# Kernel optimization log

Measured on AMD Instinct MI355X. Metric: run time of the kernel, lower is better.

Reference implementation:

```python
import jax, jax.numpy as jnp
import numpy as np

B, S, T, E, H = 16, 96, 50, 128, 128
D2 = 2 * H
V = 32000
NGRAM = 2
ALPHA = 0.25


def _lstm(x, Wih, Whh, b, reverse=False):
    # x: [N, T, E] -> outputs [N, T, H], final h, c (PyTorch gate order i,f,g,o)
    xt = jnp.swapaxes(x, 0, 1)
    if reverse:
        xt = xt[::-1]
    n = x.shape[0]
    h = Whh.shape[1]
    init = (jnp.zeros((n, h), x.dtype), jnp.zeros((n, h), x.dtype))

    def step(carry, xin):
        hprev, cprev = carry
        g = xin @ Wih.T + hprev @ Whh.T + b
        i, f, gg, o = jnp.split(g, 4, axis=-1)
        c = jax.nn.sigmoid(f) * cprev + jax.nn.sigmoid(i) * jnp.tanh(gg)
        hnew = jax.nn.sigmoid(o) * jnp.tanh(c)
        return (hnew, c), hnew

    (hT, cT), outs = jax.lax.scan(step, init, xt)
    if reverse:
        outs = outs[::-1]
    return jnp.swapaxes(outs, 0, 1), hT, cT


def _gru(x, h, Wi, Wh, bi, bh):
    # PyTorch GRUCell, gate order r,z,n
    gi = x @ Wi.T + bi
    gh = h @ Wh.T + bh
    ir, iz, inn = jnp.split(gi, 3, axis=-1)
    hr, hz, hn = jnp.split(gh, 3, axis=-1)
    r = jax.nn.sigmoid(ir + hr)
    z = jax.nn.sigmoid(iz + hz)
    n = jnp.tanh(inn + r * hn)
    return (1.0 - z) * n + z * h


def _norm_scale(x):
    # (||x|| + alpha) / (||x|| + 1), detached as in the original
    v = jnp.linalg.norm(x, axis=1)
    return jax.lax.stop_gradient(((v + ALPHA) / (v + 1.0))[:, None])


def setup_inputs() -> dict:
    key = jax.random.key(0)
    ks = jax.random.split(key, 30)
    rn = lambda k, sh: jax.random.normal(k, sh, jnp.float32) * 0.05
    return {
        "enc_batch": jax.random.randint(ks[0], (B * S, T), 0, V),
        "struct_parent": jax.random.randint(ks[1], (B, S, S), 0, B * S + 1),
        "struct_child": jax.random.randint(ks[2], (B, S, S), 0, B * S + 1),
        "mask_emb": (jax.random.uniform(ks[3], (B, S, S, 1)) < 0.2).astype(jnp.float32),
        "emb_table": rn(ks[4], (V, E)),
        "Wih_f": rn(ks[5], (4 * H, E)), "Whh_f": rn(ks[6], (4 * H, H)), "b_f": rn(ks[7], (4 * H,)),
        "Wih_b": rn(ks[8], (4 * H, E)), "Whh_b": rn(ks[9], (4 * H, H)), "b_b": rn(ks[10], (4 * H,)),
        "Wc": rn(ks[11], (H, D2)), "bc": rn(ks[12], (H,)),
        "Whr": rn(ks[13], (H, D2)), "bhr": rn(ks[14], (H,)),
        "Wi_cp": rn(ks[15], (3 * D2, D2)), "Wh_cp": rn(ks[16], (3 * D2, D2)),
        "bi_cp": rn(ks[17], (3 * D2,)), "bh_cp": rn(ks[18], (3 * D2,)),
        "Wi_pc": rn(ks[19], (3 * D2, D2)), "Wh_pc": rn(ks[20], (3 * D2, D2)),
        "bi_pc": rn(ks[21], (3 * D2,)), "bh_pc": rn(ks[22], (3 * D2,)),
    }


def reference(enc_batch, struct_parent, struct_child, mask_emb, emb_table,
              Wih_f, Whh_f, b_f, Wih_b, Whh_b, b_b, Wc, bc, Whr, bhr,
              Wi_cp, Wh_cp, bi_cp, bh_cp, Wi_pc, Wh_pc, bi_pc, bh_pc):
    # Sentence encoder (bidirectional LSTM); dropout=0 -> identity
    emb = emb_table[enc_batch]                       # [B*S, T, E]
    _, hf, cf = _lstm(emb, Wih_f, Whh_f, b_f)
    _, hb, cb = _lstm(emb, Wih_b, Whh_b, b_b, reverse=True)
    c_red = jax.nn.relu(jnp.concatenate([cf, cb], 1) @ Wc.T + bc)
    h_red = jax.nn.relu(jnp.concatenate([hf, hb], 1) @ Whr.T + bhr)
    enc_states = jnp.concatenate([c_red, h_red], 1)  # [B*S, 2H]
    zero = jnp.zeros((1, D2), enc_states.dtype)
    hidden = jnp.concatenate([zero, enc_states], 0)  # [B*S+1, 2H]; row 0 = zero_emb

    # child -> parent message passing
    for _ in range(NGRAM):
        p = hidden[struct_parent].reshape(-1, D2)    # gather [B*S*S, 2H]
        c = hidden[struct_child].reshape(-1, D2)
        ch = _gru(c, p, Wi_cp, Wh_cp, bi_cp, bh_cp).reshape(B, S, S, D2)
        ch = (ch * mask_emb).sum(1).reshape(B * S, D2)
        ch = jnp.concatenate([zero, ch], 0)
        hidden = hidden + ch * _norm_scale(ch)

    # parent -> child message passing
    for _ in range(NGRAM):
        p = hidden[struct_parent].reshape(-1, D2)
        c = hidden[struct_child].reshape(-1, D2)
        ch = _gru(p, c, Wi_pc, Wh_pc, bi_pc, bh_pc).reshape(B, S, S, D2)
        ch = (ch * mask_emb).sum(2).reshape(B * S, D2)
        ch = jnp.concatenate([zero, ch], 0)
        hidden = hidden + ch * _norm_scale(ch)

    return hidden
```

## Files before the change

kernel.cpp:

```cpp
#include <hip/hip_runtime.h>

typedef unsigned short u16;
typedef __attribute__((ext_vector_type(8))) short bf8;
typedef __attribute__((ext_vector_type(4))) short s16x4;
typedef __attribute__((ext_vector_type(4))) float f32x4;
typedef __attribute__((ext_vector_type(4))) int   i32x4;
typedef __attribute__((ext_vector_type(2))) int   i32x2;

#define S_   96
#define T_   50
#define NSEQ 1536
#define NR   1537
#define XROW 520

__device__ __forceinline__ float bf2f(u16 u){ return __uint_as_float(((unsigned)u)<<16); }
__device__ __forceinline__ u16 f2bf(float f){
  unsigned u = __float_as_uint(f);
  u += 0x7fffu + ((u>>16)&1u);
  return (u16)(u>>16);
}
__device__ __forceinline__ int cvtpk(float lo, float hi){
  int r; asm("v_cvt_pk_bf16_f32 %0, %1, %2" : "=v"(r) : "v"(lo), "v"(hi)); return r;
}
__device__ __forceinline__ float sigm(float x){
  return __builtin_amdgcn_rcpf(1.f + __expf(-x));
}
__device__ __forceinline__ float tanh_(float x){
  return 1.f - 2.f*__builtin_amdgcn_rcpf(__expf(2.f*x) + 1.f);
}
__device__ __forceinline__ void bar_lds(){
  asm volatile("s_waitcnt lgkmcnt(0)\n\ts_barrier" ::: "memory");
}

struct CvtArgs { const float* s[10]; u16* d[10]; };
__global__ __launch_bounds__(256) void prep_kernel(CvtArgs a,
    const int* __restrict__ par, const int* __restrict__ chi,
    const float* __restrict__ mask,
    int2* __restrict__ ent0, int* __restrict__ cnt0,
    int2* __restrict__ ent1, int* __restrict__ cnt1)
{
  if (blockIdx.x < 1088){
    int e = (blockIdx.x*256 + threadIdx.x)*4;
    if (e >= 1114112) return;
    int t, off;
    if (e < 262144){ t = e>>16; off = e & 65535; }
    else if (e < 327680){ int e2=e-262144; t = 4+(e2>>15); off = e2&32767; }
    else { int e3=e-327680; t = 6 + e3/196608; off = e3%196608; }
    int src = off;
    if (t < 4){
      int colp = off>>7, k = off&127;
      int orig = ((colp>>4)&3)*128 + ((colp>>6)<<4) + (colp&15);
      src = orig*128 + k;
    }
    f32x4 v = *reinterpret_cast<const f32x4*>(a.s[t]+src);
    i32x2 o;
    o[0] = cvtpk(v[0], v[1]);
    o[1] = cvtpk(v[2], v[3]);
    *reinterpret_cast<i32x2*>(a.d[t]+off) = o;
  } else {
    const int rr = blockIdx.x - 1088;
    __shared__ int c0s, c1s;
    if (threadIdx.x==0){ c0s=0; c1s=0; }
    __syncthreads();
    const int l = threadIdx.x;
    if (l < S_){
      const int b = rr/S_, fx = rr%S_, base = b*S_*S_;
      int idx = base + l*S_ + fx;
      if (mask[idx] != 0.f){
        int p = atomicAdd(&c0s, 1);
        ent0[rr*S_ + p] = make_int2(chi[idx], par[idx]);
      }
      int jdx = base + fx*S_ + l;
      if (mask[jdx] != 0.f){
        int p = atomicAdd(&c1s, 1);
        ent1[rr*S_ + p] = make_int2(par[jdx], chi[jdx]);
      }
    }
    __syncthreads();
    if (threadIdx.x==0){ cnt0[rr]=c0s; cnt1[rr]=c1s; }
  }
}

__global__ __launch_bounds__(512, 2) void lstm_kernel(
    const int* __restrict__ enc, const float* __restrict__ emb,
    const u16* __restrict__ WihF, const u16* __restrict__ WhhF, const float* __restrict__ bF,
    const u16* __restrict__ WihB, const u16* __restrict__ WhhB, const float* __restrict__ bB,
    u16* __restrict__ c_cat, u16* __restrict__ h_cat)
{
  __shared__ short xh[16*XROW];
  __shared__ int   toks[16*T_];

  const int tid  = threadIdx.x;
  const int wave = tid>>6;
  const int lane = tid&63;
  const int dir  = blockIdx.y;
  const int s0   = blockIdx.x*16;

  const u16* Wih = dir ? WihB : WihF;
  const u16* Whh = dir ? WhhB : WhhF;
  const float* bb = dir ? bB  : bF;

  for (int i=tid; i<16*T_; i+=512)
    toks[i] = enc[(s0 + i/T_)*T_ + (i%T_)];

  const int mL   = lane&15;
  const int quad = lane>>4;
  const int kb   = quad*8;

  bf8 Breg[4][8];
  f32x4 bias4[4];
  #pragma unroll
  for (int n=0;n<4;n++){
    int colp = wave*64 + n*16 + mL;
    bias4[n] = *reinterpret_cast<const f32x4*>(bb + n*128 + wave*16 + quad*4);
    #pragma unroll
    for (int ks=0;ks<8;ks++){
      int k = ks*32 + kb;
      const u16* p = (k<128) ? (Wih + colp*128 + k) : (Whh + colp*128 + (k-128));
      Breg[n][ks] = *reinterpret_cast<const bf8*>(p);
      asm volatile("" : "+v"(Breg[n][ks]));
    }
  }

  if (tid<256){
    int r = tid>>4, c = tid&15;
    *reinterpret_cast<i32x4*>(&xh[r*XROW + 256 + c*8]) = (i32x4){0,0,0,0};
  }

  const int srow = tid>>5, schunk = tid&31;
  float cst[4] = {0.f,0.f,0.f,0.f};
  float hst[4] = {0.f,0.f,0.f,0.f};

  __syncthreads();

  {
    int tok0 = toks[srow*T_ + (dir ? (T_-1) : 0)];
    f32x4 x0 = *reinterpret_cast<const f32x4*>(emb + tok0*128 + schunk*4);
    int tok1 = toks[srow*T_ + (dir ? (T_-2) : 1)];
    f32x4 x1 = *reinterpret_cast<const f32x4*>(emb + tok1*128 + schunk*4);
    i32x2 p0; p0[0]=cvtpk(x0[0],x0[1]); p0[1]=cvtpk(x0[2],x0[3]);
    i32x2 p1; p1[0]=cvtpk(x1[0],x1[1]); p1[1]=cvtpk(x1[2],x1[3]);
    *reinterpret_cast<i32x2*>(&xh[srow*XROW +       schunk*4]) = p0;
    *reinterpret_cast<i32x2*>(&xh[srow*XROW + 128 + schunk*4]) = p1;
  }
  f32x4 xvA, xvB;
  {
    int tA = toks[srow*T_ + (dir ? (T_-3) : 2)];
    xvA = *reinterpret_cast<const f32x4*>(emb + tA*128 + schunk*4);
    int tB = toks[srow*T_ + (dir ? (T_-4) : 3)];
    xvB = *reinterpret_cast<const f32x4*>(emb + tB*128 + schunk*4);
  }
  __syncthreads();

  f32x4 accx[4];
  #pragma unroll
  for (int n=0;n<4;n++) accx[n] = (f32x4){0.f,0.f,0.f,0.f};
  #pragma unroll
  for (int ks=0;ks<4;ks++){
    bf8 b = *reinterpret_cast<const bf8*>(&xh[mL*XROW + ks*32 + kb]);
    #pragma unroll
    for (int n=0;n<4;n++)
      accx[n] = __builtin_amdgcn_mfma_f32_16x16x32_bf16(Breg[n][ks], b, accx[n], 0,0,0);
  }
  bar_lds();

  for (int t=0;t<T_;t++){
    const int cb = t&1, nb = cb^1;

    f32x4 acc[4];
    #pragma unroll
    for (int n=0;n<4;n++) acc[n] = accx[n];
    #pragma unroll
    for (int ks=0;ks<4;ks++){
      bf8 b = *reinterpret_cast<const bf8*>(&xh[mL*XROW + 256 + cb*128 + ks*32 + kb]);
      #pragma unroll
      for (int n=0;n<4;n++)
        acc[n] = __builtin_amdgcn_mfma_f32_16x16x32_bf16(Breg[n][4+ks], b, acc[n], 0,0,0);
    }

    if (t+2 < T_){
      i32x2 p; p[0]=cvtpk(xvA[0],xvA[1]); p[1]=cvtpk(xvA[2],xvA[3]);
      *reinterpret_cast<i32x2*>(&xh[srow*XROW + cb*128 + schunk*4]) = p;
    }
    xvA = xvB;
    if (t+4 < T_){
      int tok = toks[srow*T_ + (dir ? (T_-5-t) : (t+4))];
      xvB = *reinterpret_cast<const f32x4*>(emb + tok*128 + schunk*4);
    }

    if (t+1 < T_){
      #pragma unroll
      for (int n=0;n<4;n++) accx[n] = (f32x4){0.f,0.f,0.f,0.f};
      #pragma unroll
      for (int ks=0;ks<4;ks++){
        bf8 b = *reinterpret_cast<const bf8*>(&xh[mL*XROW + nb*128 + ks*32 + kb]);
        #pragma unroll
        for (int n=0;n<4;n++)
          accx[n] = __builtin_amdgcn_mfma_f32_16x16x32_bf16(Breg[n][ks], b, accx[n], 0,0,0);
      }
    }

    float hv4[4];
    #pragma unroll
    for (int i=0;i<4;i++){
      float gi_ = acc[0][i]+bias4[0][i];
      float gf_ = acc[1][i]+bias4[1][i];
      float gg_ = acc[2][i]+bias4[2][i];
      float go_ = acc[3][i]+bias4[3][i];
      float c = sigm(gf_)*cst[i] + sigm(gi_)*tanh_(gg_);
      float h = sigm(go_)*tanh_(c);
      cst[i]=c; hst[i]=h; hv4[i]=h;
    }
    i32x2 hp;
    hp[0]=cvtpk(hv4[0],hv4[1]); hp[1]=cvtpk(hv4[2],hv4[3]);
    *reinterpret_cast<i32x2*>(&xh[mL*XROW + 256 + nb*128 + wave*16 + quad*4]) = hp;
    bar_lds();
  }

  {
    const int ch = wave*16 + quad*4;
    const int gs = s0 + mL;
    i32x2 cp_, hp_;
    cp_[0]=cvtpk(cst[0],cst[1]); cp_[1]=cvtpk(cst[2],cst[3]);
    hp_[0]=cvtpk(hst[0],hst[1]); hp_[1]=cvtpk(hst[2],hst[3]);
    *reinterpret_cast<i32x2*>(c_cat + gs*256 + dir*128 + ch) = cp_;
    *reinterpret_cast<i32x2*>(h_cat + gs*256 + dir*128 + ch) = hp_;
  }
}

__global__ __launch_bounds__(256) void reduce_kernel(
    const u16* __restrict__ c_cat, const u16* __restrict__ h_cat,
    const u16* __restrict__ Wc, const float* __restrict__ bc,
    const u16* __restrict__ Whr, const float* __restrict__ bhr,
    float* __restrict__ hidf, u16* __restrict__ hidb)
{
  const int tid=threadIdx.x, wave=tid>>6, lane=tid&63;
  const int mL=lane&15, quad=lane>>4, kb=quad*8;
  const int m0 = blockIdx.x*64;
  const u16* A    = (wave<2) ? c_cat : h_cat;
  const u16* W    = (wave<2) ? Wc  : Whr;
  const float* bv = (wave<2) ? bc  : bhr;
  const int nb    = (wave&1)*64;
  const int obase = (wave<2) ? 0 : 128;

  f32x4 acc[4][4];
  #pragma unroll
  for (int mt=0;mt<4;mt++)
    #pragma unroll
    for (int nt=0;nt<4;nt++) acc[mt][nt] = (f32x4){0.f,0.f,0.f,0.f};

  #pragma unroll
  for (int ks=0;ks<8;ks++){
    int k = ks*32 + kb;
    bf8 bfr[4];
    #pragma unroll
    for (int nt=0;nt<4;nt++)
      bfr[nt] = *reinterpret_cast<const bf8*>(W + (nb+nt*16+mL)*256 + k);
    #pragma unroll
    for (int mt=0;mt<4;mt++){
      bf8 a = *reinterpret_cast<const bf8*>(A + (m0+mt*16+mL)*256 + k);
      #pragma unroll
      for (int nt=0;nt<4;nt++)
        acc[mt][nt] = __builtin_amdgcn_mfma_f32_16x16x32_bf16(a, bfr[nt], acc[mt][nt], 0,0,0);
    }
  }
  const int row0 = quad*4;
  float biasv[4];
  #pragma unroll
  for (int nt=0;nt<4;nt++) biasv[nt] = bv[nb+nt*16+mL];
  #pragma unroll
  for (int mt=0;mt<4;mt++){
    #pragma unroll
    for (int nt=0;nt<4;nt++){
      int col = obase + nb + nt*16 + mL;
      #pragma unroll
      for (int i=0;i<4;i++){
        int r = m0 + mt*16 + row0 + i;
        float v = fmaxf(acc[mt][nt][i] + biasv[nt], 0.f);
        hidf[(r+1)*256 + col] = v;
        hidb[(r+1)*256 + col] = f2bf(v);
      }
    }
  }
  if (blockIdx.x==0 && tid<64){
    #pragma unroll
    for (int j=0;j<4;j++){ hidf[tid*4+j] = 0.f; hidb[tid*4+j] = 0; }
  }
}

__global__ __launch_bounds__(256) void gates_gemm_kernel(
    const u16* __restrict__ hidb,
    const u16* __restrict__ Wi, const u16* __restrict__ Wh,
    const float* __restrict__ bi, const float* __restrict__ bh,
    u16* __restrict__ gi, u16* __restrict__ gh)
{
  const int tid=threadIdx.x, wave=tid>>6, lane=tid&63;
  const int mL=lane&15, quad=lane>>4, kb=quad*8;
  const int m0 = blockIdx.x*32;
  const int n0 = blockIdx.y*256 + wave*64;
  const bool isI = (n0 < 768);
  const u16* W    = isI ? Wi : Wh;
  const float* bv = isI ? bi : bh;
  u16* out        = isI ? gi : gh;
  const int nbc   = isI ? n0 : (n0-768);

  int arow[2];
  #pragma unroll
  for (int mt=0;mt<2;mt++) arow[mt] = min(m0+mt*16+mL, NR-1);

  f32x4 acc[2][4];
  #pragma unroll
  for (int mt=0;mt<2;mt++)
    #pragma unroll
    for (int nt=0;nt<4;nt++) acc[mt][nt] = (f32x4){0.f,0.f,0.f,0.f};

  #pragma unroll
  for (int ks=0;ks<8;ks++){
    int k = ks*32 + kb;
    bf8 bfr[4];
    #pragma unroll
    for (int nt=0;nt<4;nt++)
      bfr[nt] = *reinterpret_cast<const bf8*>(W + (nbc+nt*16+mL)*256 + k);
    #pragma unroll
    for (int mt=0;mt<2;mt++){
      bf8 a = *reinterpret_cast<const bf8*>(hidb + arow[mt]*256 + k);
      #pragma unroll
      for (int nt=0;nt<4;nt++)
        acc[mt][nt] = __builtin_amdgcn_mfma_f32_16x16x32_bf16(a, bfr[nt], acc[mt][nt], 0,0,0);
    }
  }
  const int row0 = quad*4;
  float biasv[4];
  #pragma unroll
  for (int nt=0;nt<4;nt++) biasv[nt] = bv[nbc+nt*16+mL];
  #pragma unroll
  for (int mt=0;mt<2;mt++){
    #pragma unroll
    for (int nt=0;nt<4;nt++){
      #pragma unroll
      for (int i=0;i<4;i++){
        int r = m0 + mt*16 + row0 + i;
        if (r < NR)
          out[r*768 + nbc + nt*16 + mL] = f2bf(acc[mt][nt][i] + biasv[nt]);
      }
    }
  }
}

__global__ __launch_bounds__(512) void pair_kernel(
    const u16* __restrict__ gi, const u16* __restrict__ gh,
    const float* __restrict__ hin,
    float* __restrict__ hout, u16* __restrict__ bout, float* __restrict__ dout,
    const int2* __restrict__ ent, const int* __restrict__ cnt)
{
  const int r = blockIdx.x;
  const int tid = threadIdx.x, wave = tid>>6, lane = tid&63;
  __shared__ float part[8][260];
  __shared__ float ssum[4];
  if (r==0){
    if (tid<256){
      hout[tid]=0.f; bout[tid]=0;
      if (dout) dout[tid]=0.f;
    }
    return;
  }
  const int rr = r-1;
  const int n  = cnt[rr];
  const int2* e = ent + rr*S_;
  const int ch0 = lane*4;

  float a0=0.f, a1=0.f, a2=0.f, a3=0.f;
  for (int k=wave; k<n; k+=8){
    int2 pr = e[k];
    const u16* gx = gi + pr.x*768 + ch0;
    const u16* gy = gh + pr.y*768 + ch0;
    s16x4 vi0 = *reinterpret_cast<const s16x4*>(gx);
    s16x4 vi1 = *reinterpret_cast<const s16x4*>(gx+256);
    s16x4 vi2 = *reinterpret_cast<const s16x4*>(gx+512);
    s16x4 vh0 = *reinterpret_cast<const s16x4*>(gy);
    s16x4 vh1 = *reinterpret_cast<const s16x4*>(gy+256);
    s16x4 vh2 = *reinterpret_cast<const s16x4*>(gy+512);
    f32x4 hv  = *reinterpret_cast<const f32x4*>(hin + pr.y*256 + ch0);
    float o[4];
    #pragma unroll
    for (int i=0;i<4;i++){
      float rg = sigm(bf2f((u16)vi0[i]) + bf2f((u16)vh0[i]));
      float zg = sigm(bf2f((u16)vi1[i]) + bf2f((u16)vh1[i]));
      float ng = tanh_(bf2f((u16)vi2[i]) + rg*bf2f((u16)vh2[i]));
      o[i] = (1.f-zg)*ng + zg*hv[i];
    }
    a0 += o[0]; a1 += o[1]; a2 += o[2]; a3 += o[3];
  }
  *reinterpret_cast<f32x4*>(&part[wave][ch0]) = (f32x4){a0,a1,a2,a3};
  __syncthreads();

  if (tid < 256){
    float tot = part[0][tid] + part[1][tid] + part[2][tid] + part[3][tid]
              + part[4][tid] + part[5][tid] + part[6][tid] + part[7][tid];
    part[0][tid] = tot;
    float sq = tot*tot;
    #pragma unroll
    for (int off=32; off>0; off>>=1) sq += __shfl_xor(sq, off, 64);
    if (lane==0) ssum[wave] = sq;
  }
  __syncthreads();
  if (tid < 256){
    float tot = part[0][tid];
    float v  = sqrtf(ssum[0]+ssum[1]+ssum[2]+ssum[3]);
    float sc = (v + 0.25f)*__builtin_amdgcn_rcpf(v + 1.f);
    float nv = hin[r*256 + tid] + tot*sc;
    hout[r*256 + tid] = nv;
    bout[r*256 + tid] = f2bf(nv);
    if (dout) dout[r*256 + tid] = nv;
  }
}

extern "C" void kernel_launch(void* const* d_in, const int* in_sizes, int n_in,
                              void* d_out, int out_size, void* d_ws, size_t ws_size,
                              hipStream_t stream)
{
  const int*   enc  = (const int*)  d_in[0];
  const int*   spar = (const int*)  d_in[1];
  const int*   schi = (const int*)  d_in[2];
  const float* mask = (const float*)d_in[3];
  const float* emb  = (const float*)d_in[4];
  const float* WihF = (const float*)d_in[5];
  const float* WhhF = (const float*)d_in[6];
  const float* bF   = (const float*)d_in[7];
  const float* WihB = (const float*)d_in[8];
  const float* WhhB = (const float*)d_in[9];
  const float* bB   = (const float*)d_in[10];
  const float* Wc   = (const float*)d_in[11];
  const float* bc   = (const float*)d_in[12];
  const float* Whr  = (const float*)d_in[13];
  const float* bhr  = (const float*)d_in[14];
  const float* WiCP = (const float*)d_in[15];
  const float* WhCP = (const float*)d_in[16];
  const float* biCP = (const float*)d_in[17];
  const float* bhCP = (const float*)d_in[18];
  const float* WiPC = (const float*)d_in[19];
  const float* WhPC = (const float*)d_in[20];
  const float* biPC = (const float*)d_in[21];
  const float* bhPC = (const float*)d_in[22];

  char* ws = (char*)d_ws;
  u16*   c_cat = (u16*)  (ws + 0);
  u16*   h_cat = (u16*)  (ws + 786432);
  float* hf0   = (float*)(ws + 1572864);
  float* hf1   = (float*)(ws + 3146752);
  u16*   hb    = (u16*)  (ws + 4720640);
  u16*   gi    = (u16*)  (ws + 5507584);
  u16*   gh    = (u16*)  (ws + 7868416);
  u16*   wbf   = (u16*)  (ws + 10229248);
  int2*  ent0  = (int2*) (ws + 12457472);
  int2*  ent1  = (int2*) (ws + 13637120);
  int*   cnt0  = (int*)  (ws + 14816768);
  int*   cnt1  = (int*)  (ws + 14822912);
  float* out   = (float*)d_out;

  u16* bWihF = wbf + 0;
  u16* bWhhF = wbf + 65536;
  u16* bWihB = wbf + 131072;
  u16* bWhhB = wbf + 196608;
  u16* bWc   = wbf + 262144;
  u16* bWhr  = wbf + 294912;
  u16* bWiCP = wbf + 327680;
  u16* bWhCP = wbf + 524288;
  u16* bWiPC = wbf + 720896;
  u16* bWhPC = wbf + 917504;

  CvtArgs ca;
  ca.s[0]=WihF; ca.s[1]=WhhF; ca.s[2]=WihB; ca.s[3]=WhhB;
  ca.s[4]=Wc;   ca.s[5]=Whr;
  ca.s[6]=WiCP; ca.s[7]=WhCP; ca.s[8]=WiPC; ca.s[9]=WhPC;
  ca.d[0]=bWihF; ca.d[1]=bWhhF; ca.d[2]=bWihB; ca.d[3]=bWhhB;
  ca.d[4]=bWc;   ca.d[5]=bWhr;
  ca.d[6]=bWiCP; ca.d[7]=bWhCP; ca.d[8]=bWiPC; ca.d[9]=bWhPC;
  prep_kernel<<<dim3(1088+NSEQ), dim3(256), 0, stream>>>(
      ca, spar, schi, mask, ent0, cnt0, ent1, cnt1);

  lstm_kernel<<<dim3(96,2), dim3(512), 0, stream>>>(
      enc, emb, bWihF,bWhhF,bF, bWihB,bWhhB,bB, c_cat, h_cat);
  reduce_kernel<<<dim3(24), dim3(256), 0, stream>>>(
      c_cat,h_cat, bWc,bc,bWhr,bhr, hf0,hb);

  float* hfb[2] = {hf0,hf1};
  int cur = 0;
  for (int it=0; it<4; it++){
    const u16* Wi   = (it<2)?bWiCP:bWiPC;
    const u16* Wh   = (it<2)?bWhCP:bWhPC;
    const float* bi = (it<2)?biCP:biPC;
    const float* bh = (it<2)?bhCP:bhPC;
    int nxt = cur^1;
    gates_gemm_kernel<<<dim3(49,6), dim3(256), 0, stream>>>(
        hb, Wi,Wh,bi,bh, gi,gh);
    pair_kernel<<<dim3(NR), dim3(512), 0, stream>>>(
        gi,gh, hfb[cur], hfb[nxt], hb,
        (it==3)?out:(float*)nullptr,
        (it<2)?ent0:ent1, (it<2)?cnt0:cnt1);
    cur = nxt;
  }
}
```

Measured before the change: 322.2 us.

## Merge forward and backward LSTM directions into one 1024-thread block

```diff
diff --git a/kernel.cpp b/kernel.cpp
--- a/kernel.cpp
+++ b/kernel.cpp
@@ -81,26 +81,29 @@
   }
 }
 
-__global__ __launch_bounds__(512, 2) void lstm_kernel(
+__global__ __launch_bounds__(1024, 4) void lstm_kernel(
     const int* __restrict__ enc, const float* __restrict__ emb,
     const u16* __restrict__ WihF, const u16* __restrict__ WhhF, const float* __restrict__ bF,
     const u16* __restrict__ WihB, const u16* __restrict__ WhhB, const float* __restrict__ bB,
     u16* __restrict__ c_cat, u16* __restrict__ h_cat)
 {
-  __shared__ short xh[16*XROW];
+  __shared__ short xh[32*XROW];
   __shared__ int   toks[16*T_];
 
   const int tid  = threadIdx.x;
   const int wave = tid>>6;
   const int lane = tid&63;
-  const int dir  = blockIdx.y;
+  const int dir  = wave>>3;
+  const int w8   = wave&7;
   const int s0   = blockIdx.x*16;
+
+  short* X = xh + dir*16*XROW;
 
   const u16* Wih = dir ? WihB : WihF;
   const u16* Whh = dir ? WhhB : WhhF;
   const float* bb = dir ? bB  : bF;
 
-  for (int i=tid; i<16*T_; i+=512)
+  for (int i=tid; i<16*T_; i+=1024)
     toks[i] = enc[(s0 + i/T_)*T_ + (i%T_)];
 
   const int mL   = lane&15;
@@ -111,8 +114,8 @@
   f32x4 bias4[4];
   #pragma unroll
   for (int n=0;n<4;n++){
-    int colp = wave*64 + n*16 + mL;
-    bias4[n] = *reinterpret_cast<const f32x4*>(bb + n*128 + wave*16 + quad*4);
+    int colp = w8*64 + n*16 + mL;
+    bias4[n] = *reinterpret_cast<const f32x4*>(bb + n*128 + w8*16 + quad*4);
     #pragma unroll
     for (int ks=0;ks<8;ks++){
       int k = ks*32 + kb;
@@ -122,12 +125,13 @@
     }
   }
 
-  if (tid<256){
-    int r = tid>>4, c = tid&15;
-    *reinterpret_cast<i32x4*>(&xh[r*XROW + 256 + c*8]) = (i32x4){0,0,0,0};
-  }
-
-  const int srow = tid>>5, schunk = tid&31;
+  if (tid<512){
+    int d2 = tid>>8, r = (tid>>4)&15, c = tid&15;
+    *reinterpret_cast<i32x4*>(&xh[d2*16*XROW + r*XROW + 256 + c*8]) = (i32x4){0,0,0,0};
+  }
+
+  const int tid9   = tid & 511;
+  const int srow   = tid9>>5, schunk = tid9&31;
   float cst[4] = {0.f,0.f,0.f,0.f};
   float hst[4] = {0.f,0.f,0.f,0.f};
 
@@ -140,8 +144,8 @@
     f32x4 x1 = *reinterpret_cast<const f32x4*>(emb + tok1*128 + schunk*4);
     i32x2 p0; p0[0]=cvtpk(x0[0],x0[1]); p0[1]=cvtpk(x0[2],x0[3]);
     i32x2 p1; p1[0]=cvtpk(x1[0],x1[1]); p1[1]=cvtpk(x1[2],x1[3]);
-    *reinterpret_cast<i32x2*>(&xh[srow*XROW +       schunk*4]) = p0;
-    *reinterpret_cast<i32x2*>(&xh[srow*XROW + 128 + schunk*4]) = p1;
+    *reinterpret_cast<i32x2*>(&X[srow*XROW +       schunk*4]) = p0;
+    *reinterpret_cast<i32x2*>(&X[srow*XROW + 128 + schunk*4]) = p1;
   }
   f32x4 xvA, xvB;
   {
@@ -157,7 +161,7 @@
   for (int n=0;n<4;n++) accx[n] = (f32x4){0.f,0.f,0.f,0.f};
   #pragma unroll
   for (int ks=0;ks<4;ks++){
-    bf8 b = *reinterpret_cast<const bf8*>(&xh[mL*XROW + ks*32 + kb]);
+    bf8 b = *reinterpret_cast<const bf8*>(&X[mL*XROW + ks*32 + kb]);
     #pragma unroll
     for (int n=0;n<4;n++)
       accx[n] = __builtin_amdgcn_mfma_f32_16x16x32_bf16(Breg[n][ks], b, accx[n], 0,0,0);
@@ -172,7 +176,7 @@
     for (int n=0;n<4;n++) acc[n] = accx[n];
     #pragma unroll
     for (int ks=0;ks<4;ks++){
-      bf8 b = *reinterpret_cast<const bf8*>(&xh[mL*XROW + 256 + cb*128 + ks*32 + kb]);
+      bf8 b = *reinterpret_cast<const bf8*>(&X[mL*XROW + 256 + cb*128 + ks*32 + kb]);
       #pragma unroll
       for (int n=0;n<4;n++)
         acc[n] = __builtin_amdgcn_mfma_f32_16x16x32_bf16(Breg[n][4+ks], b, acc[n], 0,0,0);
@@ -180,7 +184,7 @@
 
     if (t+2 < T_){
       i32x2 p; p[0]=cvtpk(xvA[0],xvA[1]); p[1]=cvtpk(xvA[2],xvA[3]);
-      *reinterpret_cast<i32x2*>(&xh[srow*XROW + cb*128 + schunk*4]) = p;
+      *reinterpret_cast<i32x2*>(&X[srow*XROW + cb*128 + schunk*4]) = p;
     }
     xvA = xvB;
     if (t+4 < T_){
@@ -193,7 +197,7 @@
       for (int n=0;n<4;n++) accx[n] = (f32x4){0.f,0.f,0.f,0.f};
       #pragma unroll
       for (int ks=0;ks<4;ks++){
-        bf8 b = *reinterpret_cast<const bf8*>(&xh[mL*XROW + nb*128 + ks*32 + kb]);
+        bf8 b = *reinterpret_cast<const bf8*>(&X[mL*XROW + nb*128 + ks*32 + kb]);
         #pragma unroll
         for (int n=0;n<4;n++)
           accx[n] = __builtin_amdgcn_mfma_f32_16x16x32_bf16(Breg[n][ks], b, accx[n], 0,0,0);
@@ -213,12 +217,12 @@
     }
     i32x2 hp;
     hp[0]=cvtpk(hv4[0],hv4[1]); hp[1]=cvtpk(hv4[2],hv4[3]);
-    *reinterpret_cast<i32x2*>(&xh[mL*XROW + 256 + nb*128 + wave*16 + quad*4]) = hp;
+    *reinterpret_cast<i32x2*>(&X[mL*XROW + 256 + nb*128 + w8*16 + quad*4]) = hp;
     bar_lds();
   }
 
   {
-    const int ch = wave*16 + quad*4;
+    const int ch = w8*16 + quad*4;
     const int gs = s0 + mL;
     i32x2 cp_, hp_;
     cp_[0]=cvtpk(cst[0],cst[1]); cp_[1]=cvtpk(cst[2],cst[3]);
@@ -479,7 +483,7 @@
   prep_kernel<<<dim3(1088+NSEQ), dim3(256), 0, stream>>>(
       ca, spar, schi, mask, ent0, cnt0, ent1, cnt1);
 
-  lstm_kernel<<<dim3(96,2), dim3(512), 0, stream>>>(
+  lstm_kernel<<<dim3(96), dim3(1024), 0, stream>>>(
       enc, emb, bWihF,bWhhF,bF, bWihB,bWhhB,bB, c_cat, h_cat);
   reduce_kernel<<<dim3(24), dim3(256), 0, stream>>>(
       c_cat,h_cat, bWc,bc,bWhr,bhr, hf0,hb);
```

Measured after the change: 758.9 us. +135.5%, slower.

## Process 32 sequences per LSTM block with two interleaved MFMA tiles

Applied to the files above, without the earlier changes.

```diff
diff --git a/kernel.cpp b/kernel.cpp
--- a/kernel.cpp
+++ b/kernel.cpp
@@ -87,20 +87,20 @@
     const u16* __restrict__ WihB, const u16* __restrict__ WhhB, const float* __restrict__ bB,
     u16* __restrict__ c_cat, u16* __restrict__ h_cat)
 {
-  __shared__ short xh[16*XROW];
-  __shared__ int   toks[16*T_];
+  __shared__ short xh[32*XROW];
+  __shared__ int   toks[32*T_];
 
   const int tid  = threadIdx.x;
   const int wave = tid>>6;
   const int lane = tid&63;
   const int dir  = blockIdx.y;
-  const int s0   = blockIdx.x*16;
+  const int s0   = blockIdx.x*32;
 
   const u16* Wih = dir ? WihB : WihF;
   const u16* Whh = dir ? WhhB : WhhF;
   const float* bb = dir ? bB  : bF;
 
-  for (int i=tid; i<16*T_; i+=512)
+  for (int i=tid; i<32*T_; i+=512)
     toks[i] = enc[(s0 + i/T_)*T_ + (i%T_)];
 
   const int mL   = lane&15;
@@ -122,109 +122,153 @@
     }
   }
 
-  if (tid<256){
+  {
     int r = tid>>4, c = tid&15;
     *reinterpret_cast<i32x4*>(&xh[r*XROW + 256 + c*8]) = (i32x4){0,0,0,0};
   }
 
-  const int srow = tid>>5, schunk = tid&31;
-  float cst[4] = {0.f,0.f,0.f,0.f};
-  float hst[4] = {0.f,0.f,0.f,0.f};
+  const int srow = tid>>4, sch = tid&15;
+  float cst0[4] = {0.f,0.f,0.f,0.f}, hst0[4] = {0.f,0.f,0.f,0.f};
+  float cst1[4] = {0.f,0.f,0.f,0.f}, hst1[4] = {0.f,0.f,0.f,0.f};
 
   __syncthreads();
 
   {
     int tok0 = toks[srow*T_ + (dir ? (T_-1) : 0)];
-    f32x4 x0 = *reinterpret_cast<const f32x4*>(emb + tok0*128 + schunk*4);
+    f32x4 a0 = *reinterpret_cast<const f32x4*>(emb + tok0*128 + sch*8);
+    f32x4 a1 = *reinterpret_cast<const f32x4*>(emb + tok0*128 + sch*8 + 4);
     int tok1 = toks[srow*T_ + (dir ? (T_-2) : 1)];
-    f32x4 x1 = *reinterpret_cast<const f32x4*>(emb + tok1*128 + schunk*4);
-    i32x2 p0; p0[0]=cvtpk(x0[0],x0[1]); p0[1]=cvtpk(x0[2],x0[3]);
-    i32x2 p1; p1[0]=cvtpk(x1[0],x1[1]); p1[1]=cvtpk(x1[2],x1[3]);
-    *reinterpret_cast<i32x2*>(&xh[srow*XROW +       schunk*4]) = p0;
-    *reinterpret_cast<i32x2*>(&xh[srow*XROW + 128 + schunk*4]) = p1;
-  }
-  f32x4 xvA, xvB;
+    f32x4 b0 = *reinterpret_cast<const f32x4*>(emb + tok1*128 + sch*8);
+    f32x4 b1 = *reinterpret_cast<const f32x4*>(emb + tok1*128 + sch*8 + 4);
+    i32x4 p0, p1;
+    p0[0]=cvtpk(a0[0],a0[1]); p0[1]=cvtpk(a0[2],a0[3]);
+    p0[2]=cvtpk(a1[0],a1[1]); p0[3]=cvtpk(a1[2],a1[3]);
+    p1[0]=cvtpk(b0[0],b0[1]); p1[1]=cvtpk(b0[2],b0[3]);
+    p1[2]=cvtpk(b1[0],b1[1]); p1[3]=cvtpk(b1[2],b1[3]);
+    *reinterpret_cast<i32x4*>(&xh[srow*XROW +       sch*8]) = p0;
+    *reinterpret_cast<i32x4*>(&xh[srow*XROW + 128 + sch*8]) = p1;
+  }
+  f32x4 xvA0, xvA1, xvB0, xvB1;
   {
     int tA = toks[srow*T_ + (dir ? (T_-3) : 2)];
-    xvA = *reinterpret_cast<const f32x4*>(emb + tA*128 + schunk*4);
+    xvA0 = *reinterpret_cast<const f32x4*>(emb + tA*128 + sch*8);
+    xvA1 = *reinterpret_cast<const f32x4*>(emb + tA*128 + sch*8 + 4);
     int tB = toks[srow*T_ + (dir ? (T_-4) : 3)];
-    xvB = *reinterpret_cast<const f32x4*>(emb + tB*128 + schunk*4);
+    xvB0 = *reinterpret_cast<const f32x4*>(emb + tB*128 + sch*8);
+    xvB1 = *reinterpret_cast<const f32x4*>(emb + tB*128 + sch*8 + 4);
   }
   __syncthreads();
 
-  f32x4 accx[4];
-  #pragma unroll
-  for (int n=0;n<4;n++) accx[n] = (f32x4){0.f,0.f,0.f,0.f};
+  f32x4 accx0[4], accx1[4];
+  #pragma unroll
+  for (int n=0;n<4;n++){ accx0[n] = (f32x4){0.f,0.f,0.f,0.f};
+                         accx1[n] = (f32x4){0.f,0.f,0.f,0.f}; }
   #pragma unroll
   for (int ks=0;ks<4;ks++){
-    bf8 b = *reinterpret_cast<const bf8*>(&xh[mL*XROW + ks*32 + kb]);
-    #pragma unroll
-    for (int n=0;n<4;n++)
-      accx[n] = __builtin_amdgcn_mfma_f32_16x16x32_bf16(Breg[n][ks], b, accx[n], 0,0,0);
+    bf8 b0 = *reinterpret_cast<const bf8*>(&xh[ mL     *XROW + ks*32 + kb]);
+    bf8 b1 = *reinterpret_cast<const bf8*>(&xh[(16+mL)*XROW + ks*32 + kb]);
+    #pragma unroll
+    for (int n=0;n<4;n++){
+      accx0[n] = __builtin_amdgcn_mfma_f32_16x16x32_bf16(Breg[n][ks], b0, accx0[n], 0,0,0);
+      accx1[n] = __builtin_amdgcn_mfma_f32_16x16x32_bf16(Breg[n][ks], b1, accx1[n], 0,0,0);
+    }
   }
   bar_lds();
 
   for (int t=0;t<T_;t++){
     const int cb = t&1, nb = cb^1;
 
-    f32x4 acc[4];
-    #pragma unroll
-    for (int n=0;n<4;n++) acc[n] = accx[n];
+    f32x4 acc0[4], acc1[4];
+    #pragma unroll
+    for (int n=0;n<4;n++){ acc0[n] = accx0[n]; acc1[n] = accx1[n]; }
     #pragma unroll
     for (int ks=0;ks<4;ks++){
-      bf8 b = *reinterpret_cast<const bf8*>(&xh[mL*XROW + 256 + cb*128 + ks*32 + kb]);
-      #pragma unroll
-      for (int n=0;n<4;n++)
-        acc[n] = __builtin_amdgcn_mfma_f32_16x16x32_bf16(Breg[n][4+ks], b, acc[n], 0,0,0);
+      bf8 b0 = *reinterpret_cast<const bf8*>(&xh[ mL     *XROW + 256 + cb*128 + ks*32 + kb]);
+      bf8 b1 = *reinterpret_cast<const bf8*>(&xh[(16+mL)*XROW + 256 + cb*128 + ks*32 + kb]);
+      #pragma unroll
+      for (int n=0;n<4;n++){
+        acc0[n] = __builtin_amdgcn_mfma_f32_16x16x32_bf16(Breg[n][4+ks], b0, acc0[n], 0,0,0);
+        acc1[n] = __builtin_amdgcn_mfma_f32_16x16x32_bf16(Breg[n][4+ks], b1, acc1[n], 0,0,0);
+      }
     }
 
     if (t+2 < T_){
-      i32x2 p; p[0]=cvtpk(xvA[0],xvA[1]); p[1]=cvtpk(xvA[2],xvA[3]);
-      *reinterpret_cast<i32x2*>(&xh[srow*XROW + cb*128 + schunk*4]) = p;
-    }
-    xvA = xvB;
+      i32x4 p;
+      p[0]=cvtpk(xvA0[0],xvA0[1]); p[1]=cvtpk(xvA0[2],xvA0[3]);
+      p[2]=cvtpk(xvA1[0],xvA1[1]); p[3]=cvtpk(xvA1[2],xvA1[3]);
+      *reinterpret_cast<i32x4*>(&xh[srow*XROW + cb*128 + sch*8]) = p;
+    }
+    xvA0 = xvB0; xvA1 = xvB1;
     if (t+4 < T_){
       int tok = toks[srow*T_ + (dir ? (T_-5-t) : (t+4))];
-      xvB = *reinterpret_cast<const f32x4*>(emb + tok*128 + schunk*4);
+      xvB0 = *reinterpret_cast<const f32x4*>(emb + tok*128 + sch*8);
+      xvB1 = *reinterpret_cast<const f32x4*>(emb + tok*128 + sch*8 + 4);
     }
 
     if (t+1 < T_){
       #pragma unroll
-      for (int n=0;n<4;n++) accx[n] = (f32x4){0.f,0.f,0.f,0.f};
+      for (int n=0;n<4;n++){ accx0[n] = (f32x4){0.f,0.f,0.f,0.f};
+                             accx1[n] = (f32x4){0.f,0.f,0.f,0.f}; }
       #pragma unroll
       for (int ks=0;ks<4;ks++){
-        bf8 b = *reinterpret_cast<const bf8*>(&xh[mL*XROW + nb*128 + ks*32 + kb]);
+        bf8 b0 = *reinterpret_cast<const bf8*>(&xh[ mL     *XROW + nb*128 + ks*32 + kb]);
+        bf8 b1 = *reinterpret_cast<const bf8*>(&xh[(16+mL)*XROW + nb*128 + ks*32 + kb]);
         #pragma unroll
-        for (int n=0;n<4;n++)
-          accx[n] = __builtin_amdgcn_mfma_f32_16x16x32_bf16(Breg[n][ks], b, accx[n], 0,0,0);
-      }
-    }
-
-    float hv4[4];
-    #pragma unroll
-    for (int i=0;i<4;i++){
-      float gi_ = acc[0][i]+bias4[0][i];
-      float gf_ = acc[1][i]+bias4[1][i];
-      float gg_ = acc[2][i]+bias4[2][i];
-      float go_ = acc[3][i]+bias4[3][i];
-      float c = sigm(gf_)*cst[i] + sigm(gi_)*tanh_(gg_);
-      float h = sigm(go_)*tanh_(c);
-      cst[i]=c; hst[i]=h; hv4[i]=h;
-    }
-    i32x2 hp;
-    hp[0]=cvtpk(hv4[0],hv4[1]); hp[1]=cvtpk(hv4[2],hv4[3]);
-    *reinterpret_cast<i32x2*>(&xh[mL*XROW + 256 + nb*128 + wave*16 + quad*4]) = hp;
+        for (int n=0;n<4;n++){
+          accx0[n] = __builtin_amdgcn_mfma_f32_16x16x32_bf16(Breg[n][ks], b0, accx0[n], 0,0,0);
+          accx1[n] = __builtin_amdgcn_mfma_f32_16x16x32_bf16(Breg[n][ks], b1, accx1[n], 0,0,0);
+        }
+      }
+    }
+
+    {
+      float hv4[4];
+      #pragma unroll
+      for (int i=0;i<4;i++){
+        float gi_ = acc0[0][i]+bias4[0][i];
+        float gf_ = acc0[1][i]+bias4[1][i];
+        float gg_ = acc0[2][i]+bias4[2][i];
+        float go_ = acc0[3][i]+bias4[3][i];
+        float c = sigm(gf_)*cst0[i] + sigm(gi_)*tanh_(gg_);
+        float h = sigm(go_)*tanh_(c);
+        cst0[i]=c; hst0[i]=h; hv4[i]=h;
+      }
+      i32x2 hp;
+      hp[0]=cvtpk(hv4[0],hv4[1]); hp[1]=cvtpk(hv4[2],hv4[3]);
+      *reinterpret_cast<i32x2*>(&xh[mL*XROW + 256 + nb*128 + wave*16 + quad*4]) = hp;
+    }
+    {
+      float hv4[4];
+      #pragma unroll
+      for (int i=0;i<4;i++){
+        float gi_ = acc1[0][i]+bias4[0][i];
+        float gf_ = acc1[1][i]+bias4[1][i];
+        float gg_ = acc1[2][i]+bias4[2][i];
+        float go_ = acc1[3][i]+bias4[3][i];
+        float c = sigm(gf_)*cst1[i] + sigm(gi_)*tanh_(gg_);
+        float h = sigm(go_)*tanh_(c);
+        cst1[i]=c; hst1[i]=h; hv4[i]=h;
+      }
+      i32x2 hp;
+      hp[0]=cvtpk(hv4[0],hv4[1]); hp[1]=cvtpk(hv4[2],hv4[3]);
+      *reinterpret_cast<i32x2*>(&xh[(16+mL)*XROW + 256 + nb*128 + wave*16 + quad*4]) = hp;
+    }
     bar_lds();
   }
 
   {
     const int ch = wave*16 + quad*4;
-    const int gs = s0 + mL;
     i32x2 cp_, hp_;
-    cp_[0]=cvtpk(cst[0],cst[1]); cp_[1]=cvtpk(cst[2],cst[3]);
-    hp_[0]=cvtpk(hst[0],hst[1]); hp_[1]=cvtpk(hst[2],hst[3]);
-    *reinterpret_cast<i32x2*>(c_cat + gs*256 + dir*128 + ch) = cp_;
-    *reinterpret_cast<i32x2*>(h_cat + gs*256 + dir*128 + ch) = hp_;
+    int gs0 = s0 + mL;
+    cp_[0]=cvtpk(cst0[0],cst0[1]); cp_[1]=cvtpk(cst0[2],cst0[3]);
+    hp_[0]=cvtpk(hst0[0],hst0[1]); hp_[1]=cvtpk(hst0[2],hst0[3]);
+    *reinterpret_cast<i32x2*>(c_cat + gs0*256 + dir*128 + ch) = cp_;
+    *reinterpret_cast<i32x2*>(h_cat + gs0*256 + dir*128 + ch) = hp_;
+    int gs1 = s0 + 16 + mL;
+    cp_[0]=cvtpk(cst1[0],cst1[1]); cp_[1]=cvtpk(cst1[2],cst1[3]);
+    hp_[0]=cvtpk(hst1[0],hst1[1]); hp_[1]=cvtpk(hst1[2],hst1[3]);
+    *reinterpret_cast<i32x2*>(c_cat + gs1*256 + dir*128 + ch) = cp_;
+    *reinterpret_cast<i32x2*>(h_cat + gs1*256 + dir*128 + ch) = hp_;
   }
 }
 
@@ -479,7 +523,7 @@
   prep_kernel<<<dim3(1088+NSEQ), dim3(256), 0, stream>>>(
       ca, spar, schi, mask, ent0, cnt0, ent1, cnt1);
 
-  lstm_kernel<<<dim3(96,2), dim3(512), 0, stream>>>(
+  lstm_kernel<<<dim3(48,2), dim3(512), 0, stream>>>(
       enc, emb, bWihF,bWhhF,bF, bWihB,bWhhB,bB, c_cat, h_cat);
   reduce_kernel<<<dim3(24), dim3(256), 0, stream>>>(
       c_cat,h_cat, bWc,bc,bWhr,bhr, hf0,hb);
```

Result: slower. 376.5 us (+16.9%).

## Remap pair_kernel to one wavefront per row, removing shared-memory reduction

Applied to the files above, without the earlier changes.

```diff
diff --git a/kernel.cpp b/kernel.cpp
--- a/kernel.cpp
+++ b/kernel.cpp
@@ -353,66 +353,89 @@
     float* __restrict__ hout, u16* __restrict__ bout, float* __restrict__ dout,
     const int2* __restrict__ ent, const int* __restrict__ cnt)
 {
-  const int r = blockIdx.x;
-  const int tid = threadIdx.x, wave = tid>>6, lane = tid&63;
-  __shared__ float part[8][260];
-  __shared__ float ssum[4];
-  if (r==0){
-    if (tid<256){
-      hout[tid]=0.f; bout[tid]=0;
-      if (dout) dout[tid]=0.f;
+  const int wave = threadIdx.x>>6, lane = threadIdx.x&63;
+  const int r = blockIdx.x*8 + wave;
+  if (r >= NR) return;
+  const int ch0 = lane*4;
+
+  if (r == 0){
+    #pragma unroll
+    for (int j=0;j<4;j++){
+      hout[ch0+j]=0.f; bout[ch0+j]=0;
+      if (dout) dout[ch0+j]=0.f;
     }
     return;
   }
   const int rr = r-1;
   const int n  = cnt[rr];
   const int2* e = ent + rr*S_;
-  const int ch0 = lane*4;
-
-  float a0=0.f, a1=0.f, a2=0.f, a3=0.f;
-  for (int k=wave; k<n; k+=8){
-    int2 pr = e[k];
-    const u16* gx = gi + pr.x*768 + ch0;
-    const u16* gy = gh + pr.y*768 + ch0;
-    s16x4 vi0 = *reinterpret_cast<const s16x4*>(gx);
-    s16x4 vi1 = *reinterpret_cast<const s16x4*>(gx+256);
-    s16x4 vi2 = *reinterpret_cast<const s16x4*>(gx+512);
-    s16x4 vh0 = *reinterpret_cast<const s16x4*>(gy);
-    s16x4 vh1 = *reinterpret_cast<const s16x4*>(gy+256);
-    s16x4 vh2 = *reinterpret_cast<const s16x4*>(gy+512);
-    f32x4 hv  = *reinterpret_cast<const f32x4*>(hin + pr.y*256 + ch0);
-    float o[4];
-    #pragma unroll
-    for (int i=0;i<4;i++){
-      float rg = sigm(bf2f((u16)vi0[i]) + bf2f((u16)vh0[i]));
-      float zg = sigm(bf2f((u16)vi1[i]) + bf2f((u16)vh1[i]));
-      float ng = tanh_(bf2f((u16)vi2[i]) + rg*bf2f((u16)vh2[i]));
-      o[i] = (1.f-zg)*ng + zg*hv[i];
-    }
-    a0 += o[0]; a1 += o[1]; a2 += o[2]; a3 += o[3];
-  }
-  *reinterpret_cast<f32x4*>(&part[wave][ch0]) = (f32x4){a0,a1,a2,a3};
-  __syncthreads();
-
-  if (tid < 256){
-    float tot = part[0][tid] + part[1][tid] + part[2][tid] + part[3][tid]
-              + part[4][tid] + part[5][tid] + part[6][tid] + part[7][tid];
-    part[0][tid] = tot;
-    float sq = tot*tot;
-    #pragma unroll
-    for (int off=32; off>0; off>>=1) sq += __shfl_xor(sq, off, 64);
-    if (lane==0) ssum[wave] = sq;
-  }
-  __syncthreads();
-  if (tid < 256){
-    float tot = part[0][tid];
-    float v  = sqrtf(ssum[0]+ssum[1]+ssum[2]+ssum[3]);
-    float sc = (v + 0.25f)*__builtin_amdgcn_rcpf(v + 1.f);
-    float nv = hin[r*256 + tid] + tot*sc;
-    hout[r*256 + tid] = nv;
-    bout[r*256 + tid] = f2bf(nv);
-    if (dout) dout[r*256 + tid] = nv;
-  }
+
+  float a[8][4];
+  #pragma unroll
+  for (int j=0;j<8;j++){
+    #pragma unroll
+    for (int i=0;i<4;i++) a[j][i] = 0.f;
+  }
+
+  for (int k=0;k<n;k+=8){
+    #pragma unroll
+    for (int j=0;j<8;j++){
+      if (k+j < n){
+        int2 pr = e[k+j];
+        const u16* gx = gi + pr.x*768 + ch0;
+        const u16* gy = gh + pr.y*768 + ch0;
+        s16x4 vi0 = *reinterpret_cast<const s16x4*>(gx);
+        s16x4 vi1 = *reinterpret_cast<const s16x4*>(gx+256);
+        s16x4 vi2 = *reinterpret_cast<const s16x4*>(gx+512);
+        s16x4 vh0 = *reinterpret_cast<const s16x4*>(gy);
+        s16x4 vh1 = *reinterpret_cast<const s16x4*>(gy+256);
+        s16x4 vh2 = *reinterpret_cast<const s16x4*>(gy+512);
+        f32x4 hv  = *reinterpret_cast<const f32x4*>(hin + pr.y*256 + ch0);
+        #pragma unroll
+        for (int i=0;i<4;i++){
+          float rg = sigm(bf2f((u16)vi0[i]) + bf2f((u16)vh0[i]));
+          float zg = sigm(bf2f((u16)vi1[i]) + bf2f((u16)vh1[i]));
+          float ng = tanh_(bf2f((u16)vi2[i]) + rg*bf2f((u16)vh2[i]));
+          a[j][i] += (1.f-zg)*ng + zg*hv[i];
+        }
+      }
+    }
+  }
+
+  float tot[4];
+  #pragma unroll
+  for (int i=0;i<4;i++){
+    float t = a[0][i];
+    #pragma unroll
+    for (int j=1;j<8;j++) t += a[j][i];
+    tot[i] = t;
+  }
+
+  float sq[4];
+  #pragma unroll
+  for (int i=0;i<4;i++) sq[i] = tot[i]*tot[i];
+  #pragma unroll
+  for (int off=8; off>0; off>>=1){
+    #pragma unroll
+    for (int i=0;i<4;i++) sq[i] += __shfl_xor(sq[i], off, 64);
+  }
+  float ssum = (sq[0]+sq[2]) + (sq[1]+sq[3]);
+  float g0 = __shfl(ssum,  0, 64);
+  float g1 = __shfl(ssum, 16, 64);
+  float g2 = __shfl(ssum, 32, 64);
+  float g3 = __shfl(ssum, 48, 64);
+  float v  = sqrtf(((g0+g1)+g2)+g3);
+  float sc = (v + 0.25f)*__builtin_amdgcn_rcpf(v + 1.f);
+
+  f32x4 hv = *reinterpret_cast<const f32x4*>(hin + r*256 + ch0);
+  f32x4 nv;
+  #pragma unroll
+  for (int i=0;i<4;i++) nv[i] = hv[i] + tot[i]*sc;
+  *reinterpret_cast<f32x4*>(hout + r*256 + ch0) = nv;
+  i32x2 bp;
+  bp[0] = cvtpk(nv[0],nv[1]); bp[1] = cvtpk(nv[2],nv[3]);
+  *reinterpret_cast<i32x2*>(bout + r*256 + ch0) = bp;
+  if (dout) *reinterpret_cast<f32x4*>(dout + r*256 + ch0) = nv;
 }
 
 extern "C" void kernel_launch(void* const* d_in, const int* in_sizes, int n_in,
@@ -494,7 +517,7 @@
     int nxt = cur^1;
     gates_gemm_kernel<<<dim3(49,6), dim3(256), 0, stream>>>(
         hb, Wi,Wh,bi,bh, gi,gh);
-    pair_kernel<<<dim3(NR), dim3(512), 0, stream>>>(
+    pair_kernel<<<dim3(193), dim3(512), 0, stream>>>(
         gi,gh, hfb[cur], hfb[nxt], hb,
         (it==3)?out:(float*)nullptr,
         (it<2)?ent0:ent1, (it<2)?cnt0:cnt1);
```

Measured after the change: 381.0 us. +18.2%, slower.
